# Kernel tuning notes

Hardware: AMD Instinct MI355X
Metric: run time of the kernel (lower is better)

Reference implementation:

```python
import jax, jax.numpy as jnp
import numpy as np

B, N, DIM = 2, 2048, 512
H = 8
DH = DIM // H
ALPHA = 1.0
DELTA = 1.0
EPS = 1e-5


def setup_inputs() -> dict:
    key = jax.random.key(0)
    ks = jax.random.split(key, 5)
    scale = 0.02
    return {
        "z": jax.random.normal(ks[0], (B, N, DIM), dtype=jnp.float32),
        "Wq": jax.random.normal(ks[1], (DIM, DIM), dtype=jnp.float32) * scale,
        "bq": jnp.zeros((DIM,), dtype=jnp.float32),
        "Wk": jax.random.normal(ks[2], (DIM, DIM), dtype=jnp.float32) * scale,
        "bk": jnp.zeros((DIM,), dtype=jnp.float32),
        "Wv": jax.random.normal(ks[3], (DIM, DIM), dtype=jnp.float32) * scale,
        "bv": jnp.zeros((DIM,), dtype=jnp.float32),
        "Wo": jax.random.normal(ks[4], (DIM, DIM), dtype=jnp.float32) * scale,
        "bo": jnp.zeros((DIM,), dtype=jnp.float32),
    }


def _split_heads(x):
    # [B, N, DIM] -> [B, H, N, DH]
    b, n, _ = x.shape
    return x.reshape(b, n, H, DH).transpose(0, 2, 1, 3)


def reference(z, Wq, bq, Wk, bk, Wv, bv, Wo, bo):
    Q = _split_heads(z @ Wq + bq)
    K = _split_heads(z @ Wk + bk)
    V = _split_heads(z @ Wv + bv)

    # QK^T once; reuse for both the score and the squared-distance expansion
    qk = jnp.einsum("bhnd,bhmd->bhnm", Q, K)  # [B,H,N,N]

    # NeuroFocal deviation NF(Q): per-query scalar
    mu_q = Q.mean(axis=-1, keepdims=True)
    var_q = ((Q - mu_q) ** 2).mean(axis=-1, keepdims=True)
    sigma_q = jnp.sqrt(var_q + EPS)
    nf_q = jnp.abs(Q - mu_q).sum(axis=-1, keepdims=True) / (sigma_q + EPS)  # [B,H,N,1]

    # ||Q - K||^2 = |Q|^2 + |K|^2 - 2 QK^T (same math as explicit diff tensor)
    q2 = (Q ** 2).sum(axis=-1)  # [B,H,N]
    k2 = (K ** 2).sum(axis=-1)  # [B,H,N]
    omega = q2[..., :, None] + k2[..., None, :] - 2.0 * qk  # [B,H,N,N]
    omega = omega / (jnp.exp(-DELTA * nf_q) + 1.0)

    logits = qk / jnp.sqrt(jnp.float32(DH)) - ALPHA * omega
    A = jax.nn.softmax(logits, axis=-1)

    out = jnp.einsum("bhnm,bhmd->bhnd", A, V)  # [B,H,N,DH]
    out = out.transpose(0, 2, 1, 3).reshape(z.shape[0], z.shape[1], DIM)
    return out @ Wo + bo
```

## Files before the change

### kernel.cpp

```cpp
#include <hip/hip_runtime.h>
#include <hip/hip_bf16.h>

#define HH 8
#define NNq 2048
#define EPSF 1e-5f
#define LOG2E 1.4426950408889634f

typedef __bf16 bf16x8 __attribute__((ext_vector_type(8)));
typedef float f32x4 __attribute__((ext_vector_type(4)));

typedef const __attribute__((address_space(1))) unsigned int* gas_t;
typedef __attribute__((address_space(3))) unsigned int* las_t;

__device__ __forceinline__ void async16(const void* g, void* l) {
  __builtin_amdgcn_global_load_lds((gas_t)g, (las_t)l, 16, 0, 0);
}
__device__ __forceinline__ void async4(const void* g, void* l) {
  __builtin_amdgcn_global_load_lds((gas_t)g, (las_t)l, 4, 0, 0);
}

__device__ __forceinline__ unsigned short f2bf(float f) {
  union { float f; unsigned int u; } a;
  a.f = f;
  unsigned int r = a.u + 0x7fffu + ((a.u >> 16) & 1u);
  return (unsigned short)(r >> 16);
}

__global__ __launch_bounds__(256) void prep_kernel(
    const float* __restrict__ z, const float* __restrict__ W0,
    const float* __restrict__ W1, const float* __restrict__ W2,
    const float* __restrict__ W3, unsigned short* __restrict__ zb,
    unsigned short* __restrict__ Wt, unsigned int* __restrict__ k2max) {
  __shared__ float Tl[64][68];
  const int t = threadIdx.x;
  const int bx = blockIdx.x;
  if (bx < 1024) {
    const int i = (bx * 256 + t) * 8;
    const float4 a = *(const float4*)&z[i];
    const float4 b = *(const float4*)&z[i + 4];
    union { unsigned short us[8]; uint4 v; } o;
    o.us[0] = f2bf(a.x); o.us[1] = f2bf(a.y); o.us[2] = f2bf(a.z); o.us[3] = f2bf(a.w);
    o.us[4] = f2bf(b.x); o.us[5] = f2bf(b.y); o.us[6] = f2bf(b.z); o.us[7] = f2bf(b.w);
    *(uint4*)&zb[i] = o.v;
  } else if (bx < 1280) {
    const int idx0 = bx - 1024;
    const int wsel = idx0 >> 6, rem = idx0 & 63;
    const int k0 = (rem >> 3) * 64, n0 = (rem & 7) * 64;
    const float* W = (wsel == 0) ? W0 : (wsel == 1) ? W1 : (wsel == 2) ? W2 : W3;
    unsigned short* dst = Wt + (size_t)wsel * 262144;
#pragma unroll
    for (int i = 0; i < 4; ++i) {
      const int idx = t + 256 * i;
      const int row = idx >> 4, cq = (idx & 15) * 4;
      *(float4*)&Tl[row][cq] = *(const float4*)&W[(size_t)(k0 + row) * 512 + n0 + cq];
    }
    __syncthreads();
#pragma unroll
    for (int i = 0; i < 4; ++i) {
      const int idx = t + 256 * i;
      const int nr = idx >> 4, kq = (idx & 15) * 4;
      ushort4 o;
      o.x = f2bf(Tl[kq + 0][nr]);
      o.y = f2bf(Tl[kq + 1][nr]);
      o.z = f2bf(Tl[kq + 2][nr]);
      o.w = f2bf(Tl[kq + 3][nr]);
      *(ushort4*)&dst[(size_t)(n0 + nr) * 512 + k0 + kq] = o;
    }
  } else {
    k2max[t] = 0u;
  }
}

__global__ __launch_bounds__(256) void gemm_qkv(
    const unsigned short* __restrict__ A, const unsigned short* __restrict__ Wt3,
    const float* __restrict__ bq, const float* __restrict__ bk,
    const float* __restrict__ bvv, unsigned short* __restrict__ Qb,
    unsigned short* __restrict__ Ksw, unsigned short* __restrict__ Vsw,
    float* __restrict__ c1a, float* __restrict__ dva, float* __restrict__ k2a,
    float* __restrict__ q2a, unsigned int* __restrict__ k2max) {
  __shared__ __align__(16) unsigned short S[12288];
  __shared__ float wmax[4];

  const int which = blockIdx.z;
  const unsigned short* Wt = Wt3 + (size_t)which * 262144;
  const float* bias = (which == 0) ? bq : (which == 1) ? bk : bvv;

  const int t = threadIdx.x;
  const int w = t >> 6, lane = t & 63, ln = lane & 15, quad = lane >> 4;
  const int r0 = blockIdx.x * 128, h = blockIdx.y;
  const int c0 = h * 64;
  const int b = r0 >> 11, n0 = r0 & 2047;
  const int bh = b * HH + h;

  f32x4 acc[2][4];
#pragma unroll
  for (int rf = 0; rf < 2; ++rf)
#pragma unroll
    for (int nt = 0; nt < 4; ++nt) acc[rf][nt] = (f32x4)(0.0f);

  const int lr = lane >> 3, lc = (lane & 7) * 8;

  for (int k0 = 0; k0 < 512; k0 += 64) {
#pragma unroll
    for (int i = 0; i < 4; ++i)
      async16(A + (size_t)(r0 + w * 32 + i * 8 + lr) * 512 + k0 + lc,
              S + (w * 32 + i * 8) * 64);
#pragma unroll
    for (int i = 0; i < 2; ++i)
      async16(Wt + (size_t)(c0 + w * 16 + i * 8 + lr) * 512 + k0 + lc,
              S + 8192 + (w * 16 + i * 8) * 64);
    __syncthreads();
#pragma unroll
    for (int kk = 0; kk < 64; kk += 32) {
      bf16x8 af[2];
#pragma unroll
      for (int rf = 0; rf < 2; ++rf)
        af[rf] = *(const bf16x8*)&S[(w * 32 + rf * 16 + ln) * 64 + kk + quad * 8];
#pragma unroll
      for (int nt = 0; nt < 4; ++nt) {
        const bf16x8 bf = *(const bf16x8*)&S[8192 + (nt * 16 + ln) * 64 + kk + quad * 8];
#pragma unroll
        for (int rf = 0; rf < 2; ++rf)
          acc[rf][nt] = __builtin_amdgcn_mfma_f32_16x16x32_bf16(af[rf], bf, acc[rf][nt], 0, 0, 0);
      }
    }
    __syncthreads();
  }

  float x[2][4][4];
#pragma unroll
  for (int nt = 0; nt < 4; ++nt) {
    const float bv = bias[c0 + nt * 16 + ln];
#pragma unroll
    for (int rf = 0; rf < 2; ++rf)
#pragma unroll
      for (int r = 0; r < 4; ++r) x[rf][nt][r] = acc[rf][nt][r] + bv;
  }

  if (which == 0) {
#pragma unroll
    for (int rf = 0; rf < 2; ++rf)
#pragma unroll
      for (int r = 0; r < 4; ++r) {
        float s1 = x[rf][0][r] + x[rf][1][r] + x[rf][2][r] + x[rf][3][r];
#pragma unroll
        for (int off = 1; off < 16; off <<= 1) s1 += __shfl_xor(s1, off, 64);
        const float mu = s1 * (1.0f / 64.0f);
        float s2 = 0.0f, sa = 0.0f;
#pragma unroll
        for (int nt = 0; nt < 4; ++nt) {
          const float dx = x[rf][nt][r] - mu;
          s2 += dx * dx;
          sa += fabsf(dx);
        }
#pragma unroll
        for (int off = 1; off < 16; off <<= 1) {
          s2 += __shfl_xor(s2, off, 64);
          sa += __shfl_xor(sa, off, 64);
        }
        if (ln == 0) {
          const float sigma = sqrtf(s2 * (1.0f / 64.0f) + EPSF);
          const float nf = sa / (sigma + EPSF);
          const float dInv = 1.0f / (__expf(-nf) + 1.0f);
          const int row = bh * NNq + n0 + w * 32 + rf * 16 + quad * 4 + r;
          c1a[row] = (0.125f + 2.0f * dInv) * LOG2E;
          dva[row] = dInv * LOG2E;
          q2a[row] = s2 + 64.0f * mu * mu;
        }
      }
#pragma unroll
    for (int rf = 0; rf < 2; ++rf)
#pragma unroll
      for (int nt = 0; nt < 4; ++nt)
#pragma unroll
        for (int r = 0; r < 4; ++r)
          S[(w * 32 + rf * 16 + quad * 4 + r) * 72 + nt * 16 + ln] = f2bf(x[rf][nt][r]);
    __syncthreads();
#pragma unroll
    for (int i = 0; i < 4; ++i) {
      const int idx = t + 256 * i;
      const int q = idx >> 3, c = idx & 7;
      *(uint4*)&Qb[((size_t)bh * NNq + n0 + q) * 64 + c * 8] =
          *(const uint4*)&S[q * 72 + c * 8];
    }
  } else if (which == 1) {
    float mx = 0.0f;
#pragma unroll
    for (int rf = 0; rf < 2; ++rf)
#pragma unroll
      for (int r = 0; r < 4; ++r) {
        float s2 = 0.0f;
#pragma unroll
        for (int nt = 0; nt < 4; ++nt) s2 += x[rf][nt][r] * x[rf][nt][r];
#pragma unroll
        for (int off = 1; off < 16; off <<= 1) s2 += __shfl_xor(s2, off, 64);
        if (ln == 0) k2a[bh * NNq + n0 + w * 32 + rf * 16 + quad * 4 + r] = s2;
        mx = fmaxf(mx, s2);
      }
#pragma unroll
    for (int off = 16; off < 64; off <<= 1) mx = fmaxf(mx, __shfl_xor(mx, off, 64));
    if (lane == 0) wmax[w] = mx;
#pragma unroll
    for (int rf = 0; rf < 2; ++rf)
#pragma unroll
      for (int nt = 0; nt < 4; ++nt) {
        const int c = nt * 2 + (ln >> 3);
#pragma unroll
        for (int r = 0; r < 4; ++r) {
          const int key = w * 32 + rf * 16 + quad * 4 + r;
          const int klo = key & 63;
          S[(key >> 6) * 4096 + klo * 64 + ((c ^ (klo & 7)) * 8) + (ln & 7)] =
              f2bf(x[rf][nt][r]);
        }
      }
    __syncthreads();
    if (t == 0) {
      const float m = fmaxf(fmaxf(wmax[0], wmax[1]), fmaxf(wmax[2], wmax[3]));
      atomicMax(&k2max[bh * 16], __float_as_uint(m));
    }
    unsigned short* dst = Ksw + ((size_t)bh * 32 + (n0 >> 6)) * 4096;
#pragma unroll
    for (int i = 0; i < 4; ++i) {
      const int idx = t + 256 * i;
      *(uint4*)&dst[idx * 8] = *(const uint4*)&S[idx * 8];
    }
  } else {
#pragma unroll
    for (int rf = 0; rf < 2; ++rf)
#pragma unroll
      for (int nt = 0; nt < 4; ++nt) {
        const int d = nt * 16 + ln;
#pragma unroll
        for (int r = 0; r < 4; ++r) {
          const int key = w * 32 + rf * 16 + quad * 4 + r;
          const int klo = key & 63;
          S[d * 128 + (key >> 6) * 64 + (((klo >> 3) ^ (d & 7)) * 8) + (klo & 7)] =
              f2bf(x[rf][nt][r]);
        }
      }
    __syncthreads();
    unsigned short* dst = Vsw + ((size_t)bh * 32 + (n0 >> 6)) * 4096;
#pragma unroll
    for (int i = 0; i < 4; ++i) {
      const int g = t + 256 * i;
      const int tile = g >> 9, d = (g >> 3) & 63, j8 = (g & 7) * 8;
      *(uint4*)&dst[tile * 4096 + d * 64 + j8] =
          *(const uint4*)&S[d * 128 + tile * 64 + j8];
    }
  }
}

__global__ __launch_bounds__(512) void attn_kernel(
    const unsigned short* __restrict__ Qb, const unsigned short* __restrict__ Ksw,
    const unsigned short* __restrict__ Vsw, const float* __restrict__ c1a,
    const float* __restrict__ dva, const float* __restrict__ k2a,
    const float* __restrict__ q2a, const unsigned int* __restrict__ k2maxu,
    unsigned short* __restrict__ attnb) {
  __shared__ __align__(16) char smem[51712];

  const int t = threadIdx.x;
  const int w8 = t >> 6, lane = t & 63, ln = lane & 15, quad = lane >> 4;
  const int half = w8 >> 2, wl = w8 & 3;
  const int qt = blockIdx.x, bh = blockIdx.y;
  const int b = bh >> 3, h = bh & 7;
  const int q0 = qt * 64;
  const int rowbase = bh * NNq;

  unsigned short* Kt = (unsigned short*)(smem + half * 16384);
  unsigned short* Vt = (unsigned short*)(smem + half * 16384 + 8192);
  unsigned short* Ps = (unsigned short*)(smem + 32768 + half * 9216);
  float* k2t = (float*)(smem + 51200 + half * 256);

  const int qg = q0 + wl * 16 + ln;
  const unsigned short* qrow = Qb + ((size_t)rowbase + qg) * 64;
  const bf16x8 aq0 = *(const bf16x8*)(qrow + quad * 8);
  const bf16x8 aq1 = *(const bf16x8*)(qrow + 32 + quad * 8);

  const float k2m = __uint_as_float(k2maxu[bh * 16]);
  const float c1q = c1a[rowbase + qg];
  const float dvq = dva[rowbase + qg];
  const float Mqq = c1q * sqrtf(q2a[rowbase + qg] * k2m);
  float L = 0.0f;
  f32x4 O[4];
#pragma unroll
  for (int nt = 0; nt < 4; ++nt) O[nt] = (f32x4)(0.0f);

  const unsigned short* Kg = Ksw + (size_t)bh * 32 * 4096;
  const unsigned short* Vg = Vsw + (size_t)bh * 32 * 4096;
  const float* k2g = k2a + rowbase + half * 1024;
  const int sw = quad ^ (ln & 7);
  const int sw1 = (4 + quad) ^ (ln & 7);

  for (int kt = 0; kt < 16; ++kt) {
    {
      const size_t tb = (size_t)(half * 16 + kt) * 4096 + wl * 1024;
      async16(Kg + tb + lane * 8, Kt + wl * 1024);
      async16(Kg + tb + 512 + lane * 8, Kt + wl * 1024 + 512);
      async16(Vg + tb + lane * 8, Vt + wl * 1024);
      async16(Vg + tb + 512 + lane * 8, Vt + wl * 1024 + 512);
      if (wl == 0) async4(k2g + kt * 64 + lane, k2t);
    }
    __syncthreads();

    f32x4 s[4];
#pragma unroll
    for (int nt = 0; nt < 4; ++nt) {
      const unsigned short* kb = Kt + (nt * 16 + ln) * 64;
      const bf16x8 b0 = *(const bf16x8*)(kb + sw * 8);
      const bf16x8 b1 = *(const bf16x8*)(kb + sw1 * 8);
      f32x4 a = (f32x4)(0.0f);
      a = __builtin_amdgcn_mfma_f32_16x16x32_bf16(b0, aq0, a, 0, 0, 0);
      a = __builtin_amdgcn_mfma_f32_16x16x32_bf16(b1, aq1, a, 0, 0, 0);
      s[nt] = a;
    }

#pragma unroll
    for (int nt = 0; nt < 4; ++nt) {
      const f32x4 k2v = *(const f32x4*)&k2t[nt * 16 + quad * 4];
      ushort4 pk;
      float p0 = __builtin_amdgcn_exp2f(c1q * s[nt][0] - dvq * k2v[0] - Mqq);
      float p1 = __builtin_amdgcn_exp2f(c1q * s[nt][1] - dvq * k2v[1] - Mqq);
      float p2 = __builtin_amdgcn_exp2f(c1q * s[nt][2] - dvq * k2v[2] - Mqq);
      float p3 = __builtin_amdgcn_exp2f(c1q * s[nt][3] - dvq * k2v[3] - Mqq);
      L += (p0 + p1) + (p2 + p3);
      pk.x = f2bf(p0); pk.y = f2bf(p1); pk.z = f2bf(p2); pk.w = f2bf(p3);
      *(ushort4*)&Ps[(wl * 16 + ln) * 72 + nt * 16 + quad * 4] = pk;
    }
    const unsigned short* pr = Ps + (wl * 16 + ln) * 72;
    const bf16x8 pa0 = *(const bf16x8*)(pr + quad * 8);
    const bf16x8 pa1 = *(const bf16x8*)(pr + 32 + quad * 8);

#pragma unroll
    for (int nt = 0; nt < 4; ++nt) {
      const unsigned short* vb = Vt + (nt * 16 + ln) * 64;
      const bf16x8 vb0 = *(const bf16x8*)(vb + sw * 8);
      const bf16x8 vb1 = *(const bf16x8*)(vb + sw1 * 8);
      O[nt] = __builtin_amdgcn_mfma_f32_16x16x32_bf16(pa0, vb0, O[nt], 0, 0, 0);
      O[nt] = __builtin_amdgcn_mfma_f32_16x16x32_bf16(pa1, vb1, O[nt], 0, 0, 0);
    }
    __syncthreads();
  }

  L += __shfl_xor(L, 16, 64);
  L += __shfl_xor(L, 32, 64);

  float* Ost = (float*)(smem + half * 16384);
  float* Lst = (float*)(smem + 32768 + half * 9216);
#pragma unroll
  for (int nt = 0; nt < 4; ++nt)
#pragma unroll
    for (int r = 0; r < 4; ++r)
      Ost[(wl * 16 + quad * 4 + r) * 64 + nt * 16 + ln] = O[nt][r];
  if (quad == 0) Lst[wl * 16 + ln] = L;
  __syncthreads();

  const float* O0 = (const float*)smem;
  const float* O1 = (const float*)(smem + 16384);
  const float* L0 = (const float*)(smem + 32768);
  const float* L1 = (const float*)(smem + 32768 + 9216);
  const int q = t >> 3, c8 = (t & 7) * 8;
  const float inv = 1.0f / (L0[q] + L1[q]);
  const int base = q * 64 + c8;
  float4 a0 = *(const float4*)&O0[base];
  float4 a1 = *(const float4*)&O0[base + 4];
  const float4 b0 = *(const float4*)&O1[base];
  const float4 b1 = *(const float4*)&O1[base + 4];
  union { unsigned short us[8]; uint4 v; } ov;
  ov.us[0] = f2bf((a0.x + b0.x) * inv);
  ov.us[1] = f2bf((a0.y + b0.y) * inv);
  ov.us[2] = f2bf((a0.z + b0.z) * inv);
  ov.us[3] = f2bf((a0.w + b0.w) * inv);
  ov.us[4] = f2bf((a1.x + b1.x) * inv);
  ov.us[5] = f2bf((a1.y + b1.y) * inv);
  ov.us[6] = f2bf((a1.z + b1.z) * inv);
  ov.us[7] = f2bf((a1.w + b1.w) * inv);
  *(uint4*)&attnb[((size_t)(b * NNq + q0 + q)) * 512 + h * 64 + c8] = ov.v;
}

__global__ __launch_bounds__(256) void gemm_out(
    const unsigned short* __restrict__ A, const unsigned short* __restrict__ Wt,
    const float* __restrict__ bias, float* __restrict__ of) {
  __shared__ __align__(16) unsigned short S[8192];
  __shared__ float Tl[64][68];
  const int t = threadIdx.x;
  const int w = t >> 6, lane = t & 63, ln = lane & 15, quad = lane >> 4;
  const int r0 = blockIdx.x * 64, c0 = blockIdx.y * 64;
  const int lr = lane >> 3, lc = (lane & 7) * 8;

  f32x4 acc[4];
#pragma unroll
  for (int nt = 0; nt < 4; ++nt) acc[nt] = (f32x4)(0.0f);

  for (int k0 = 0; k0 < 512; k0 += 64) {
#pragma unroll
    for (int i = 0; i < 2; ++i) {
      async16(A + (size_t)(r0 + w * 16 + i * 8 + lr) * 512 + k0 + lc,
              S + (w * 16 + i * 8) * 64);
      async16(Wt + (size_t)(c0 + w * 16 + i * 8 + lr) * 512 + k0 + lc,
              S + 4096 + (w * 16 + i * 8) * 64);
    }
    __syncthreads();
#pragma unroll
    for (int kk = 0; kk < 64; kk += 32) {
      const bf16x8 af = *(const bf16x8*)&S[(w * 16 + ln) * 64 + kk + quad * 8];
#pragma unroll
      for (int nt = 0; nt < 4; ++nt) {
        const bf16x8 bf = *(const bf16x8*)&S[4096 + (nt * 16 + ln) * 64 + kk + quad * 8];
        acc[nt] = __builtin_amdgcn_mfma_f32_16x16x32_bf16(af, bf, acc[nt], 0, 0, 0);
      }
    }
    __syncthreads();
  }
#pragma unroll
  for (int nt = 0; nt < 4; ++nt) {
    const float bv = bias[c0 + nt * 16 + ln];
#pragma unroll
    for (int r = 0; r < 4; ++r)
      Tl[w * 16 + quad * 4 + r][nt * 16 + ln] = acc[nt][r] + bv;
  }
  __syncthreads();
#pragma unroll
  for (int i = 0; i < 4; ++i) {
    const int idx = t + 256 * i;
    const int row = idx >> 4, c4 = (idx & 15) * 4;
    *(float4*)&of[(size_t)(r0 + row) * 512 + c0 + c4] = *(const float4*)&Tl[row][c4];
  }
}

extern "C" void kernel_launch(void* const* d_in, const int* in_sizes, int n_in,
                              void* d_out, int out_size, void* d_ws,
                              size_t ws_size, hipStream_t stream) {
  const float* z = (const float*)d_in[0];
  const float* Wq = (const float*)d_in[1];
  const float* bq = (const float*)d_in[2];
  const float* Wk = (const float*)d_in[3];
  const float* bk = (const float*)d_in[4];
  const float* Wv = (const float*)d_in[5];
  const float* bv = (const float*)d_in[6];
  const float* Wo = (const float*)d_in[7];
  const float* bo = (const float*)d_in[8];
  float* out = (float*)d_out;

  char* ws = (char*)d_ws;
  unsigned short* zb = (unsigned short*)(ws);
  unsigned short* Wt = (unsigned short*)(ws + 4194304);
  unsigned short* Qb = (unsigned short*)(ws + 6291456);
  unsigned short* Ksw = (unsigned short*)(ws + 10485760);
  unsigned short* Vsw = (unsigned short*)(ws + 14680064);
  float* c1 = (float*)(ws + 18874368);
  float* dv = (float*)(ws + 19005440);
  float* k2 = (float*)(ws + 19136512);
  float* q2 = (float*)(ws + 19267584);
  unsigned short* attnb = (unsigned short*)(ws + 19398656);
  unsigned int* k2max = (unsigned int*)(ws + 23592960);

  hipLaunchKernelGGL(prep_kernel, dim3(1281), dim3(256), 0, stream, z, Wq, Wk,
                     Wv, Wo, zb, Wt, k2max);
  hipLaunchKernelGGL(gemm_qkv, dim3(32, 8, 3), dim3(256), 0, stream, zb, Wt,
                     bq, bk, bv, Qb, Ksw, Vsw, c1, dv, k2, q2, k2max);
  hipLaunchKernelGGL(attn_kernel, dim3(32, 16), dim3(512), 0, stream, Qb, Ksw,
                     Vsw, c1, dv, k2, q2, k2max, attnb);
  hipLaunchKernelGGL(gemm_out, dim3(64, 8), dim3(256), 0, stream, attnb,
                     Wt + 786432, bo, out);
}
```

Baseline: 142.4 us.

## Swizzle GEMM operand layouts, widen K tiles, preload k2 row into LDS

Stores bf16 z, transposed weights and the attention output with an XOR swizzle of 8-element chunks within each 64-column group, so the GEMM LDS fragment reads avoid bank conflicts without padding. The QKV and output GEMMs now stage 128-wide K tiles per iteration, which halves the number of loop trips and barriers at the cost of more LDS. The attention kernel loads each half's full k2 vector into LDS once instead of issuing a small load every tile, and converts probabilities with packed bf16 conversion intrinsics. The larger LDS footprint may reduce occupancy.

```diff
diff --git a/kernel.cpp b/kernel.cpp
--- a/kernel.cpp
+++ b/kernel.cpp
@@ -24,6 +24,10 @@
   a.f = f;
   unsigned int r = a.u + 0x7fffu + ((a.u >> 16) & 1u);
   return (unsigned short)(r >> 16);
+}
+
+__device__ __forceinline__ int swzk(int row, int k) {
+  return (k & ~63) | ((((k >> 3) ^ row) & 7) << 3) | (k & 7);
 }
 
 __global__ __launch_bounds__(256) void prep_kernel(
@@ -36,12 +40,13 @@
   const int bx = blockIdx.x;
   if (bx < 1024) {
     const int i = (bx * 256 + t) * 8;
+    const int row = i >> 9, k = i & 511;
     const float4 a = *(const float4*)&z[i];
     const float4 b = *(const float4*)&z[i + 4];
     union { unsigned short us[8]; uint4 v; } o;
     o.us[0] = f2bf(a.x); o.us[1] = f2bf(a.y); o.us[2] = f2bf(a.z); o.us[3] = f2bf(a.w);
     o.us[4] = f2bf(b.x); o.us[5] = f2bf(b.y); o.us[6] = f2bf(b.z); o.us[7] = f2bf(b.w);
-    *(uint4*)&zb[i] = o.v;
+    *(uint4*)&zb[(row << 9) | swzk(row, k)] = o.v;
   } else if (bx < 1280) {
     const int idx0 = bx - 1024;
     const int wsel = idx0 >> 6, rem = idx0 & 63;
@@ -64,7 +69,8 @@
       o.y = f2bf(Tl[kq + 1][nr]);
       o.z = f2bf(Tl[kq + 2][nr]);
       o.w = f2bf(Tl[kq + 3][nr]);
-      *(ushort4*)&dst[(size_t)(n0 + nr) * 512 + k0 + kq] = o;
+      const int n = n0 + nr;
+      *(ushort4*)&dst[(size_t)n * 512 + swzk(n, k0 + kq)] = o;
     }
   } else {
     k2max[t] = 0u;
@@ -78,7 +84,7 @@
     unsigned short* __restrict__ Ksw, unsigned short* __restrict__ Vsw,
     float* __restrict__ c1a, float* __restrict__ dva, float* __restrict__ k2a,
     float* __restrict__ q2a, unsigned int* __restrict__ k2max) {
-  __shared__ __align__(16) unsigned short S[12288];
+  __shared__ __align__(16) unsigned short S[24576];
   __shared__ float wmax[4];
 
   const int which = blockIdx.z;
@@ -98,27 +104,29 @@
 #pragma unroll
     for (int nt = 0; nt < 4; ++nt) acc[rf][nt] = (f32x4)(0.0f);
 
-  const int lr = lane >> 3, lc = (lane & 7) * 8;
-
-  for (int k0 = 0; k0 < 512; k0 += 64) {
+  const int lr = lane >> 4, lc = (lane & 15) * 8;
+
+  for (int k0 = 0; k0 < 512; k0 += 128) {
+#pragma unroll
+    for (int i = 0; i < 8; ++i)
+      async16(A + (size_t)(r0 + w * 32 + i * 4 + lr) * 512 + k0 + lc,
+              S + (w * 32 + i * 4) * 128);
 #pragma unroll
     for (int i = 0; i < 4; ++i)
-      async16(A + (size_t)(r0 + w * 32 + i * 8 + lr) * 512 + k0 + lc,
-              S + (w * 32 + i * 8) * 64);
-#pragma unroll
-    for (int i = 0; i < 2; ++i)
-      async16(Wt + (size_t)(c0 + w * 16 + i * 8 + lr) * 512 + k0 + lc,
-              S + 8192 + (w * 16 + i * 8) * 64);
-    __syncthreads();
-#pragma unroll
-    for (int kk = 0; kk < 64; kk += 32) {
+      async16(Wt + (size_t)(c0 + w * 16 + i * 4 + lr) * 512 + k0 + lc,
+              S + 16384 + (w * 16 + i * 4) * 128);
+    __syncthreads();
+#pragma unroll
+    for (int kk = 0; kk < 128; kk += 32) {
+      const int cp = (kk >> 3) + quad;
+      const int cs = ((cp & 8) | ((cp ^ (ln & 7)) & 7)) * 8;
       bf16x8 af[2];
 #pragma unroll
       for (int rf = 0; rf < 2; ++rf)
-        af[rf] = *(const bf16x8*)&S[(w * 32 + rf * 16 + ln) * 64 + kk + quad * 8];
+        af[rf] = *(const bf16x8*)&S[(w * 32 + rf * 16 + ln) * 128 + cs];
 #pragma unroll
       for (int nt = 0; nt < 4; ++nt) {
-        const bf16x8 bf = *(const bf16x8*)&S[8192 + (nt * 16 + ln) * 64 + kk + quad * 8];
+        const bf16x8 bf = *(const bf16x8*)&S[16384 + (nt * 16 + ln) * 128 + cs];
 #pragma unroll
         for (int rf = 0; rf < 2; ++rf)
           acc[rf][nt] = __builtin_amdgcn_mfma_f32_16x16x32_bf16(af[rf], bf, acc[rf][nt], 0, 0, 0);
@@ -256,7 +264,7 @@
     const float* __restrict__ dva, const float* __restrict__ k2a,
     const float* __restrict__ q2a, const unsigned int* __restrict__ k2maxu,
     unsigned short* __restrict__ attnb) {
-  __shared__ __align__(16) char smem[51712];
+  __shared__ __align__(16) char smem[59392];
 
   const int t = threadIdx.x;
   const int w8 = t >> 6, lane = t & 63, ln = lane & 15, quad = lane >> 4;
@@ -269,7 +277,12 @@
   unsigned short* Kt = (unsigned short*)(smem + half * 16384);
   unsigned short* Vt = (unsigned short*)(smem + half * 16384 + 8192);
   unsigned short* Ps = (unsigned short*)(smem + 32768 + half * 9216);
-  float* k2t = (float*)(smem + 51200 + half * 256);
+  float* k2h = (float*)(smem + 51200 + half * 4096);
+
+  const float* k2g = k2a + rowbase + half * 1024;
+#pragma unroll
+  for (int i = 0; i < 4; ++i)
+    async4(k2g + wl * 256 + i * 64 + lane, k2h + wl * 256 + i * 64);
 
   const int qg = q0 + wl * 16 + ln;
   const unsigned short* qrow = Qb + ((size_t)rowbase + qg) * 64;
@@ -287,7 +300,6 @@
 
   const unsigned short* Kg = Ksw + (size_t)bh * 32 * 4096;
   const unsigned short* Vg = Vsw + (size_t)bh * 32 * 4096;
-  const float* k2g = k2a + rowbase + half * 1024;
   const int sw = quad ^ (ln & 7);
   const int sw1 = (4 + quad) ^ (ln & 7);
 
@@ -298,7 +310,6 @@
       async16(Kg + tb + 512 + lane * 8, Kt + wl * 1024 + 512);
       async16(Vg + tb + lane * 8, Vt + wl * 1024);
       async16(Vg + tb + 512 + lane * 8, Vt + wl * 1024 + 512);
-      if (wl == 0) async4(k2g + kt * 64 + lane, k2t);
     }
     __syncthreads();
 
@@ -316,15 +327,17 @@
 
 #pragma unroll
     for (int nt = 0; nt < 4; ++nt) {
-      const f32x4 k2v = *(const f32x4*)&k2t[nt * 16 + quad * 4];
-      ushort4 pk;
-      float p0 = __builtin_amdgcn_exp2f(c1q * s[nt][0] - dvq * k2v[0] - Mqq);
-      float p1 = __builtin_amdgcn_exp2f(c1q * s[nt][1] - dvq * k2v[1] - Mqq);
-      float p2 = __builtin_amdgcn_exp2f(c1q * s[nt][2] - dvq * k2v[2] - Mqq);
-      float p3 = __builtin_amdgcn_exp2f(c1q * s[nt][3] - dvq * k2v[3] - Mqq);
+      const f32x4 k2v = *(const f32x4*)&k2h[kt * 64 + nt * 16 + quad * 4];
+      const float p0 = __builtin_amdgcn_exp2f(c1q * s[nt][0] - dvq * k2v[0] - Mqq);
+      const float p1 = __builtin_amdgcn_exp2f(c1q * s[nt][1] - dvq * k2v[1] - Mqq);
+      const float p2 = __builtin_amdgcn_exp2f(c1q * s[nt][2] - dvq * k2v[2] - Mqq);
+      const float p3 = __builtin_amdgcn_exp2f(c1q * s[nt][3] - dvq * k2v[3] - Mqq);
       L += (p0 + p1) + (p2 + p3);
-      pk.x = f2bf(p0); pk.y = f2bf(p1); pk.z = f2bf(p2); pk.w = f2bf(p3);
-      *(ushort4*)&Ps[(wl * 16 + ln) * 72 + nt * 16 + quad * 4] = pk;
+      union { __hip_bfloat162 h; unsigned int u; } c01, c23;
+      c01.h = __float22bfloat162_rn(make_float2(p0, p1));
+      c23.h = __float22bfloat162_rn(make_float2(p2, p3));
+      uint2 pu; pu.x = c01.u; pu.y = c23.u;
+      *(uint2*)&Ps[(wl * 16 + ln) * 72 + nt * 16 + quad * 4] = pu;
     }
     const unsigned short* pr = Ps + (wl * 16 + ln) * 72;
     const bf16x8 pa0 = *(const bf16x8*)(pr + quad * 8);
@@ -374,38 +387,43 @@
   ov.us[5] = f2bf((a1.y + b1.y) * inv);
   ov.us[6] = f2bf((a1.z + b1.z) * inv);
   ov.us[7] = f2bf((a1.w + b1.w) * inv);
-  *(uint4*)&attnb[((size_t)(b * NNq + q0 + q)) * 512 + h * 64 + c8] = ov.v;
+  const int nrow = q0 + q;
+  *(uint4*)&attnb[((size_t)(b * NNq + nrow)) * 512 + swzk(nrow, h * 64 + c8)] = ov.v;
 }
 
 __global__ __launch_bounds__(256) void gemm_out(
     const unsigned short* __restrict__ A, const unsigned short* __restrict__ Wt,
     const float* __restrict__ bias, float* __restrict__ of) {
-  __shared__ __align__(16) unsigned short S[8192];
-  __shared__ float Tl[64][68];
+  __shared__ __align__(16) char sbuf[32768];
+  unsigned short* S = (unsigned short*)sbuf;
+  float (*Tl)[68] = (float(*)[68])sbuf;
+
   const int t = threadIdx.x;
   const int w = t >> 6, lane = t & 63, ln = lane & 15, quad = lane >> 4;
   const int r0 = blockIdx.x * 64, c0 = blockIdx.y * 64;
-  const int lr = lane >> 3, lc = (lane & 7) * 8;
+  const int lr = lane >> 4, lc = (lane & 15) * 8;
 
   f32x4 acc[4];
 #pragma unroll
   for (int nt = 0; nt < 4; ++nt) acc[nt] = (f32x4)(0.0f);
 
-  for (int k0 = 0; k0 < 512; k0 += 64) {
-#pragma unroll
-    for (int i = 0; i < 2; ++i) {
-      async16(A + (size_t)(r0 + w * 16 + i * 8 + lr) * 512 + k0 + lc,
-              S + (w * 16 + i * 8) * 64);
-      async16(Wt + (size_t)(c0 + w * 16 + i * 8 + lr) * 512 + k0 + lc,
-              S + 4096 + (w * 16 + i * 8) * 64);
-    }
-    __syncthreads();
-#pragma unroll
-    for (int kk = 0; kk < 64; kk += 32) {
-      const bf16x8 af = *(const bf16x8*)&S[(w * 16 + ln) * 64 + kk + quad * 8];
+  for (int k0 = 0; k0 < 512; k0 += 128) {
+#pragma unroll
+    for (int i = 0; i < 4; ++i) {
+      async16(A + (size_t)(r0 + w * 16 + i * 4 + lr) * 512 + k0 + lc,
+              S + (w * 16 + i * 4) * 128);
+      async16(Wt + (size_t)(c0 + w * 16 + i * 4 + lr) * 512 + k0 + lc,
+              S + 8192 + (w * 16 + i * 4) * 128);
+    }
+    __syncthreads();
+#pragma unroll
+    for (int kk = 0; kk < 128; kk += 32) {
+      const int cp = (kk >> 3) + quad;
+      const int cs = ((cp & 8) | ((cp ^ (ln & 7)) & 7)) * 8;
+      const bf16x8 af = *(const bf16x8*)&S[(w * 16 + ln) * 128 + cs];
 #pragma unroll
       for (int nt = 0; nt < 4; ++nt) {
-        const bf16x8 bf = *(const bf16x8*)&S[4096 + (nt * 16 + ln) * 64 + kk + quad * 8];
+        const bf16x8 bf = *(const bf16x8*)&S[8192 + (nt * 16 + ln) * 128 + cs];
         acc[nt] = __builtin_amdgcn_mfma_f32_16x16x32_bf16(af, bf, acc[nt], 0, 0, 0);
       }
     }
```

New measurement: 135.3 us (median of 2 runs). 5.0% less time.
